# Kernel optimization log

Measured on AMD Instinct MI355X. Metric: run time of the kernel, lower is better.

The kernel has to match this reference:

```python
import jax, jax.numpy as jnp
import numpy as np

REPR_IN = (16, 16, 8)
REPR_OUT = (32, 16, 8)
NUM_BASIS = 16
MAX_RADIUS = 2.0
GAMMA = 16.0  # radial basis sharpness

def _dim(repr_):
    return sum(m * (2 * l + 1) for l, m in enumerate(repr_))

DIM_IN = _dim(REPR_IN)          # 104
SIZE_OUT = _dim(REPR_OUT)       # 120
NUM_GATES = sum(REPR_OUT[1:])   # 24
DIM_OUT = SIZE_OUT + NUM_GATES  # 144 (conv emits gates too)


def setup_inputs() -> dict:
    key = jax.random.key(0)
    k1, k2, k3, k4 = jax.random.split(key, 4)
    B, N, M = 4, 1024, 1024
    features = jax.random.normal(k1, (B, DIM_IN, M), jnp.float32)
    difference_matrix = jax.random.normal(k2, (B, N, M, 3), jnp.float32)
    relative_mask = jax.random.uniform(k3, (B, N, M), jnp.float32)
    W = jax.random.normal(k4, (NUM_BASIS, DIM_OUT, DIM_IN), jnp.float32) / np.sqrt(NUM_BASIS * DIM_IN)
    return {"features": features, "difference_matrix": difference_matrix,
            "relative_mask": relative_mask, "W": W}


def _radial_basis(diff):
    # diff: [B, N, M, 3] -> phi: [B, N, M, K]
    r = jnp.sqrt(jnp.sum(diff * diff, axis=-1) + 1e-12)
    centers = jnp.linspace(0.0, MAX_RADIUS, NUM_BASIS, dtype=diff.dtype)
    return jnp.exp(-GAMMA * jnp.square(r[..., None] - centers))


def reference(features, difference_matrix, relative_mask, W):
    # SE3PointConvolution: per-pair kernel K[b,n,m] = sum_k phi_k(|r_nm|) W[k]
    # masked by relative_mask; out[b,o,n] = sum_m K[b,n,m,o,i] feat[b,i,m].
    # Fused so the [B,N,M,144,104] kernel is never materialized.
    phi = _radial_basis(difference_matrix) * relative_mask[..., None]  # [B,N,M,K]
    tmp = jnp.einsum('bnmk,bim->bnki', phi, features)                  # [B,N,K,DIM_IN]
    y = jnp.einsum('bnki,koi->bon', tmp, W)                            # [B,DIM_OUT,N]

    B, _, N = y.shape
    # scalar (l=0) activation, bias=False
    outs = [jax.nn.relu(y[:, :REPR_OUT[0]])]
    # gates: last NUM_GATES channels, sigmoid
    g = jax.nn.sigmoid(y[:, SIZE_OUT:])
    begin_y, begin_g = REPR_OUT[0], 0
    for l, mul in enumerate(REPR_OUT):
        if l == 0 or mul == 0:
            continue
        d = 2 * l + 1
        fy = y[:, begin_y:begin_y + mul * d].reshape(B, mul, d, N)
        fg = g[:, begin_g:begin_g + mul].reshape(B, mul, 1, N)
        outs.append((fy * fg).reshape(B, mul * d, N))
        begin_y += mul * d
        begin_g += mul
    return jnp.concatenate(outs, axis=1)  # [B, SIZE_OUT, N]
```

## Files before the change

kernel.cpp:

```cpp
#include <hip/hip_runtime.h>


typedef __attribute__((ext_vector_type(4))) float f32x4;
typedef __attribute__((ext_vector_type(8))) short s16x8;

#define DI 104
#define DO 144
#define TTST 1688
#define YST 9

#define W_ELEMS 239616
#define F_ELEMS 425984

#define OFF_PHI0 0
#define OFF_PHI1 16384
#define OFF_FEAT0 32768
#define OFF_FEAT1 47104
#define OFF_Y 61440
#define SMEM_TOTAL (61440 + 144*9*4)

__device__ __forceinline__ float fexp2(float x) {
#if __has_builtin(__builtin_amdgcn_exp2f)
    return __builtin_amdgcn_exp2f(x);
#else
    return exp2f(x);
#endif
}
__device__ __forceinline__ float flog2(float x) {
#if __has_builtin(__builtin_amdgcn_logf)
    return __builtin_amdgcn_logf(x);
#else
    return log2f(x);
#endif
}
__device__ __forceinline__ float fsqrt_(float x) {
#if __has_builtin(__builtin_amdgcn_sqrtf)
    return __builtin_amdgcn_sqrtf(x);
#else
    return sqrtf(x);
#endif
}
__device__ __forceinline__ float frcp_(float x) {
#if __has_builtin(__builtin_amdgcn_rcpf)
    return __builtin_amdgcn_rcpf(x);
#else
    return 1.0f / x;
#endif
}
__device__ __forceinline__ unsigned int pkbf(float lo, float hi) {
    unsigned int a = __builtin_bit_cast(unsigned int, lo) + 0x8000u;
    unsigned int b = __builtin_bit_cast(unsigned int, hi) + 0x8000u;
    return __builtin_amdgcn_perm(b, a, 0x07060302u);
}
__device__ __forceinline__ unsigned short f2b(float f) {
    return (unsigned short)((__builtin_bit_cast(unsigned int, f) + 0x8000u) >> 16);
}

__global__ __launch_bounds__(256, 8)
void cvt_kernel(const float* __restrict__ feat_g, const float* __restrict__ W_g,
                unsigned short* __restrict__ ws)
{
    int gid = blockIdx.x * 256 + threadIdx.x;
    const float* src;
    unsigned short* dst;
    if (gid < W_ELEMS/8) {
        src = W_g + gid*8;  dst = ws + gid*8;
    } else {
        int g2 = gid - W_ELEMS/8;
        src = feat_g + g2*8; dst = ws + W_ELEMS + g2*8;
    }
    f32x4 a = *(const f32x4*)src;
    f32x4 b = *(const f32x4*)(src + 4);
    unsigned int o[4] = { pkbf(a[0],a[1]), pkbf(a[2],a[3]), pkbf(b[0],b[1]), pkbf(b[2],b[3]) };
    *(f32x4*)dst = *(f32x4*)o;
}

#define LOAD_DM(M0)                                                    \
    do {                                                               \
        const float* dp_ = diff_g + (dmrow + (M0) + pml)*3;            \
        dx0 = dp_[0]; dy0 = dp_[1]; dz0 = dp_[2];                      \
        dx1 = dp_[3]; dy1 = dp_[4]; dz1 = dp_[5];                      \
        const float* mp_ = mask_g + dmrow + (M0) + pml;                \
        mk0 = mp_[0]; mk1 = mp_[1];                                    \
    } while (0)

#define LOAD_FEAT(M0)                                                          \
    do {                                                                       \
        fr0 = *(const s16x8*)(featbf + fbase + ((size_t)fi0 << 10) + (M0) + (fj << 3)); \
        if (t < 320)                                                           \
            fr1 = *(const s16x8*)(featbf + fbase + ((size_t)fi1 << 10) + (M0) + (fj << 3)); \
    } while (0)

#define COMPUTE_WRITE_PHI(BUF)                                         \
    do {                                                               \
        unsigned short* pw_ = (BUF) + phirow;                          \
        float r0_ = fsqrt_(fmaf(dx0,dx0, fmaf(dy0,dy0, fmaf(dz0,dz0, 1e-12f)))); \
        float r1_ = fsqrt_(fmaf(dx1,dx1, fmaf(dy1,dy1, fmaf(dz1,dz1, 1e-12f)))); \
        float t0_ = r0_ - K0OFF, t1_ = r1_ - K0OFF;                    \
        float v0_ = fexp2(fmaf(CEXP*t0_, t0_, flog2(mk0)));            \
        float v1_ = fexp2(fmaf(CEXP*t1_, t1_, flog2(mk1)));            \
        float w0_ = fexp2(fmaf(A1, r0_, S0B));                         \
        float w1_ = fexp2(fmaf(A1, r1_, S0B));                         \
        *(unsigned int*)(pw_ + (pblk << 3)) = pkbf(v0_, v1_);          \
        _Pragma("unroll")                                              \
        for (int j_ = 1; j_ < 8; ++j_) {                               \
            v0_ *= w0_; w0_ *= U2;                                     \
            v1_ *= w1_; w1_ *= U2;                                     \
            *(unsigned int*)(pw_ + j_*64 + ((pblk ^ j_) << 3)) = pkbf(v0_, v1_); \
        }                                                              \
    } while (0)

#define WRITE_FEAT(BUF)                                                \
    do {                                                               \
        *(s16x8*)((BUF) + fi0*64 + fjs) = fr0;                         \
        if (t < 320) *(s16x8*)((BUF) + fi1*64 + fjs) = fr1;            \
    } while (0)

#define GEMM1(PBUF, FBUF)                                              \
    do {                                                               \
        _Pragma("unroll")                                              \
        for (int kk_ = 0; kk_ < 2; ++kk_) {                            \
            const int mo_ = ((kk_*4 + q) ^ sw) << 3;                   \
            s16x8 a0_ = *(const s16x8*)((PBUF) + ((2*wr    )*16 + l15)*64 + mo_); \
            s16x8 a1_ = *(const s16x8*)((PBUF) + ((2*wr + 1)*16 + l15)*64 + mo_); \
            _Pragma("unroll")                                          \
            for (int cc_ = 0; cc_ < 4; ++cc_) {                        \
                if (ct0 + cc_ < 7) {                                   \
                    s16x8 bf_ = *(const s16x8*)((FBUF) + ((ct0+cc_)*16 + l15)*64 + mo_); \
                    acc[0][cc_] = __builtin_amdgcn_mfma_f32_16x16x32_bf16(a0_, bf_, acc[0][cc_], 0, 0, 0); \
                    acc[1][cc_] = __builtin_amdgcn_mfma_f32_16x16x32_bf16(a1_, bf_, acc[1][cc_], 0, 0, 0); \
                }                                                      \
            }                                                          \
        }                                                              \
    } while (0)

__global__ __launch_bounds__(512, 4)
void pgb_kernel(const unsigned short* __restrict__ ws,
                const float* __restrict__ diff_g,
                const float* __restrict__ mask_g,
                float* __restrict__ out_g)
{
    const unsigned short* Wbf    = ws;
    const unsigned short* featbf = ws + W_ELEMS;

    __shared__ __align__(16) unsigned char smem[SMEM_TOTAL];
    unsigned short* Tt   = (unsigned short*)smem;
    float*          ylds = (float*)(smem + OFF_Y);
    unsigned short* phi0b  = (unsigned short*)(smem + OFF_PHI0);
    unsigned short* phi1b  = (unsigned short*)(smem + OFF_PHI1);
    unsigned short* feat0b = (unsigned short*)(smem + OFF_FEAT0);
    unsigned short* feat1b = (unsigned short*)(smem + OFF_FEAT1);

    const int t    = threadIdx.x;
    const int b    = blockIdx.x >> 7;
    const int n0   = (blockIdx.x & 127) << 3;
    const int wave = t >> 6;
    const int lane = t & 63;
    const int l15  = lane & 15;
    const int q    = lane >> 4;
    const int wr   = wave >> 1;
    const int ct0  = (wave & 1) << 2;
    const int sw   = l15 & 7;

    if (t < 256) {
        ((unsigned int*)(smem + OFF_FEAT0 + DI*128))[t] = 0u;
        ((unsigned int*)(smem + OFF_FEAT1 + DI*128))[t] = 0u;
    }

    f32x4 acc[2][4];
#pragma unroll
    for (int rr = 0; rr < 2; ++rr)
#pragma unroll
        for (int cc = 0; cc < 4; ++cc)
            acc[rr][cc] = (f32x4){0.f, 0.f, 0.f, 0.f};

    const int pn   = t >> 6;
    const int kh   = (t >> 5) & 1;
    const int pml  = (t & 31) << 1;
    const int pblk = (t & 31) >> 2;
    const int phirow = (pn*16 + kh*8)*64 + (pml & 7);
    const float CEXP = -23.083120654223414f;
    const float A1   = 6.155498841126244f;
    const float V2   = -0.8207331788168325f;
    const float U2   = fexp2(V2);
    const float K0OFF = kh ? 1.0666666666666667f : 0.f;
    const float S0B   = kh ? -6.976232019943076f : -0.41036658940841624f;
    const size_t dmrow = (size_t)((b << 10) + n0 + pn) << 10;

    const int fi0 = t >> 3, fj = t & 7;
    const int fi1 = 64 + (t >> 3);
    const int fjs = (fj ^ (fi0 & 7)) << 3;
    const size_t fbase = (size_t)b * DI << 10;

    float dx0, dy0, dz0, dx1, dy1, dz1, mk0, mk1;
    s16x8 fr0 = {}, fr1 = {};

    LOAD_DM(0);
    LOAD_FEAT(0);
    COMPUTE_WRITE_PHI(phi0b);
    WRITE_FEAT(feat0b);
    LOAD_DM(64);
    LOAD_FEAT(64);

    for (int s = 0; s < 15; ++s) {
        unsigned short* rp = (s & 1) ? phi1b  : phi0b;
        unsigned short* rf = (s & 1) ? feat1b : feat0b;
        unsigned short* wp = (s & 1) ? phi0b  : phi1b;
        unsigned short* wf = (s & 1) ? feat0b : feat1b;
        __syncthreads();
        COMPUTE_WRITE_PHI(wp);
        WRITE_FEAT(wf);
        {
            const int mnext = (s < 14 ? (s + 2) : 15) * 64;
            LOAD_DM(mnext);
            LOAD_FEAT(mnext);
        }
        GEMM1(rp, rf);
    }
    __syncthreads();
    GEMM1(phi1b, feat1b);

    __syncthreads();

#pragma unroll
    for (int rr = 0; rr < 2; ++rr) {
        int nloc = 2*wr + rr;
#pragma unroll
        for (int cc = 0; cc < 4; ++cc) {
            int i = (ct0+cc)*16 + l15;
            if (ct0 + cc < 7 && i < DI) {
#pragma unroll
                for (int r = 0; r < 4; ++r)
                    Tt[nloc*TTST + (q*4+r)*DI + i] = f2b(acc[rr][cc][r]);
            }
        }
    }
    __syncthreads();

    f32x4 y0 = (f32x4){0.f,0.f,0.f,0.f}, y1 = (f32x4){0.f,0.f,0.f,0.f};
    const int o0 = wave*16 + l15;
    const int o1 = 128 + l15;
#pragma unroll 4
    for (int s3 = 0; s3 < 52; ++s3) {
        int a = s3*4 + q;
        int k = a / 13;
        int i = (a - k*13) << 3;
        s16x8 bf = *(const s16x8*)(Tt + (l15 & 7)*TTST + s3*32 + q*8);
        s16x8 af = *(const s16x8*)(Wbf + (size_t)(k*DO + o0)*DI + i);
        y0 = __builtin_amdgcn_mfma_f32_16x16x32_bf16(af, bf, y0, 0, 0, 0);
        if (wave == 0) {
            s16x8 ag = *(const s16x8*)(Wbf + (size_t)(k*DO + o1)*DI + i);
            y1 = __builtin_amdgcn_mfma_f32_16x16x32_bf16(ag, bf, y1, 0, 0, 0);
        }
    }
    if (l15 < 8) {
#pragma unroll
        for (int r = 0; r < 4; ++r)
            ylds[(wave*16 + q*4 + r)*YST + l15] = y0[r];
        if (wave == 0) {
#pragma unroll
            for (int r = 0; r < 4; ++r)
                ylds[(128 + q*4 + r)*YST + l15] = y1[r];
        }
    }
    __syncthreads();

    const float L2E = 1.4426950408889634f;
    for (int idx = t; idx < 120*8; idx += 512) {
        int o = idx >> 3, nn = idx & 7;
        float y = ylds[o*YST + nn];
        float v;
        if (o < 32) {
            v = fmaxf(y, 0.f);
        } else if (o < 80) {
            float g = ylds[(120 + (o-32)/3)*YST + nn];
            v = y * frcp_(1.f + fexp2(-g*L2E));
        } else {
            float g = ylds[(136 + (o-80)/5)*YST + nn];
            v = y * frcp_(1.f + fexp2(-g*L2E));
        }
        out_g[((size_t)(b*120 + o) << 10) + n0 + nn] = v;
    }
}

extern "C" void kernel_launch(void* const* d_in, const int* in_sizes, int n_in,
                              void* d_out, int out_size, void* d_ws, size_t ws_size,
                              hipStream_t stream) {
    const float* feat = (const float*)d_in[0];
    const float* diff = (const float*)d_in[1];
    const float* mask = (const float*)d_in[2];
    const float* W    = (const float*)d_in[3];
    float* out = (float*)d_out;
    unsigned short* ws = (unsigned short*)d_ws;
    (void)in_sizes; (void)n_in; (void)out_size; (void)ws_size;
    cvt_kernel<<<dim3((W_ELEMS + F_ELEMS)/8/256), dim3(256), 0, stream>>>(feat, W, ws);
    pgb_kernel<<<dim3(512), dim3(512), 0, stream>>>(ws, diff, mask, out);
}
```

Before: 140.7 us.

## Single-buffer feature tile to cut LDS and raise occupancy to six blocks

Drops the double-buffered feature tile for a single buffer, shrinking shared memory, and raises the launch-bounds occupancy hint from 4 to 6 blocks per CU. The main loop is rescheduled so the next chunk's global loads are issued before the GEMM and the phi and feature writes happen after a second barrier. This aims to hide latency through more resident waves instead of software pipelining, at the cost of an extra barrier per iteration, less load/compute overlap inside a block, and tighter register limits.

```diff
diff --git a/kernel.cpp b/kernel.cpp
--- a/kernel.cpp
+++ b/kernel.cpp
@@ -14,10 +14,9 @@
 
 #define OFF_PHI0 0
 #define OFF_PHI1 16384
-#define OFF_FEAT0 32768
-#define OFF_FEAT1 47104
-#define OFF_Y 61440
-#define SMEM_TOTAL (61440 + 144*9*4)
+#define OFF_FEAT 32768
+#define OFF_Y    47104
+#define SMEM_TOTAL (47104 + 144*9*4)
 
 __device__ __forceinline__ float fexp2(float x) {
 #if __has_builtin(__builtin_amdgcn_exp2f)
@@ -134,7 +133,7 @@
         }                                                              \
     } while (0)
 
-__global__ __launch_bounds__(512, 4)
+__global__ __launch_bounds__(512, 6)
 void pgb_kernel(const unsigned short* __restrict__ ws,
                 const float* __restrict__ diff_g,
                 const float* __restrict__ mask_g,
@@ -146,10 +145,9 @@
     __shared__ __align__(16) unsigned char smem[SMEM_TOTAL];
     unsigned short* Tt   = (unsigned short*)smem;
     float*          ylds = (float*)(smem + OFF_Y);
-    unsigned short* phi0b  = (unsigned short*)(smem + OFF_PHI0);
-    unsigned short* phi1b  = (unsigned short*)(smem + OFF_PHI1);
-    unsigned short* feat0b = (unsigned short*)(smem + OFF_FEAT0);
-    unsigned short* feat1b = (unsigned short*)(smem + OFF_FEAT1);
+    unsigned short* phi0b = (unsigned short*)(smem + OFF_PHI0);
+    unsigned short* phi1b = (unsigned short*)(smem + OFF_PHI1);
+    unsigned short* featb = (unsigned short*)(smem + OFF_FEAT);
 
     const int t    = threadIdx.x;
     const int b    = blockIdx.x >> 7;
@@ -162,10 +160,7 @@
     const int ct0  = (wave & 1) << 2;
     const int sw   = l15 & 7;
 
-    if (t < 256) {
-        ((unsigned int*)(smem + OFF_FEAT0 + DI*128))[t] = 0u;
-        ((unsigned int*)(smem + OFF_FEAT1 + DI*128))[t] = 0u;
-    }
+    if (t < 256) ((unsigned int*)(smem + OFF_FEAT + DI*128))[t] = 0u;
 
     f32x4 acc[2][4];
 #pragma unroll
@@ -198,29 +193,22 @@
     LOAD_DM(0);
     LOAD_FEAT(0);
     COMPUTE_WRITE_PHI(phi0b);
-    WRITE_FEAT(feat0b);
-    LOAD_DM(64);
-    LOAD_FEAT(64);
-
-    for (int s = 0; s < 15; ++s) {
-        unsigned short* rp = (s & 1) ? phi1b  : phi0b;
-        unsigned short* rf = (s & 1) ? feat1b : feat0b;
-        unsigned short* wp = (s & 1) ? phi0b  : phi1b;
-        unsigned short* wf = (s & 1) ? feat0b : feat1b;
+    WRITE_FEAT(featb);
+
+    for (int s = 0; s < 16; ++s) {
         __syncthreads();
-        COMPUTE_WRITE_PHI(wp);
-        WRITE_FEAT(wf);
-        {
-            const int mnext = (s < 14 ? (s + 2) : 15) * 64;
-            LOAD_DM(mnext);
-            LOAD_FEAT(mnext);
-        }
-        GEMM1(rp, rf);
-    }
-    __syncthreads();
-    GEMM1(phi1b, feat1b);
-
-    __syncthreads();
+        if (s < 15) {
+            const int mn = (s + 1) << 6;
+            LOAD_DM(mn);
+            LOAD_FEAT(mn);
+        }
+        GEMM1((s & 1) ? phi1b : phi0b, featb);
+        __syncthreads();
+        if (s < 15) {
+            COMPUTE_WRITE_PHI((s & 1) ? phi0b : phi1b);
+            WRITE_FEAT(featb);
+        }
+    }
 
 #pragma unroll
     for (int rr = 0; rr < 2; ++rr) {
```

After: 182.6 us. 1.3x slower.

## Interleave radial-basis phi generation with MFMA halves and split recurrence chain

Applied to the files above, without the earlier changes.

The per-pair radial basis is now computed from an anchor that directly seeds two independent recurrences, one for basis 0-3 and one for basis 4-7, instead of one serial 7-step multiply chain. Phi writes are interleaved between the two halves of the GEMM1 k-loop so VALU/exp work overlaps the MFMA instructions within each stage. The global loads for the next stage are moved after the compute. The second recurrence seed uses a clamped power of w, which adds a few multiplies and may change rounding slightly.

```diff
diff --git a/kernel.cpp b/kernel.cpp
--- a/kernel.cpp
+++ b/kernel.cpp
@@ -91,22 +91,32 @@
             fr1 = *(const s16x8*)(featbf + fbase + ((size_t)fi1 << 10) + (M0) + (fj << 3)); \
     } while (0)
 
-#define COMPUTE_WRITE_PHI(BUF)                                         \
-    do {                                                               \
-        unsigned short* pw_ = (BUF) + phirow;                          \
+#define PHI_ANCHOR()                                                   \
+    do {                                                               \
         float r0_ = fsqrt_(fmaf(dx0,dx0, fmaf(dy0,dy0, fmaf(dz0,dz0, 1e-12f)))); \
         float r1_ = fsqrt_(fmaf(dx1,dx1, fmaf(dy1,dy1, fmaf(dz1,dz1, 1e-12f)))); \
         float t0_ = r0_ - K0OFF, t1_ = r1_ - K0OFF;                    \
-        float v0_ = fexp2(fmaf(CEXP*t0_, t0_, flog2(mk0)));            \
-        float v1_ = fexp2(fmaf(CEXP*t1_, t1_, flog2(mk1)));            \
-        float w0_ = fexp2(fmaf(A1, r0_, S0B));                         \
-        float w1_ = fexp2(fmaf(A1, r1_, S0B));                         \
-        *(unsigned int*)(pw_ + (pblk << 3)) = pkbf(v0_, v1_);          \
+        va0 = fexp2(fmaf(CEXP*t0_, t0_, flog2(mk0)));                  \
+        va1 = fexp2(fmaf(CEXP*t1_, t1_, flog2(mk1)));                  \
+        wa0 = fexp2(fmaf(A1, r0_, S0B));                               \
+        wa1 = fexp2(fmaf(A1, r1_, S0B));                               \
+        float p0_ = wa0*wa0, p1_ = wa1*wa1;                            \
+        float q0_ = fminf(p0_*p0_, 3.0e38f);                           \
+        float q1_ = fminf(p1_*p1_, 3.0e38f);                           \
+        vb0 = va0 * q0_ * U2_6;                                        \
+        vb1 = va1 * q1_ * U2_6;                                        \
+        wb0 = wa0 * U2_4;                                              \
+        wb1 = wa1 * U2_4;                                              \
+    } while (0)
+
+#define PHI_WRITE_Q(BUF, V0, V1, W0, W1, J0)                           \
+    do {                                                               \
+        unsigned short* pw_ = (BUF) + phirow;                          \
         _Pragma("unroll")                                              \
-        for (int j_ = 1; j_ < 8; ++j_) {                               \
-            v0_ *= w0_; w0_ *= U2;                                     \
-            v1_ *= w1_; w1_ *= U2;                                     \
-            *(unsigned int*)(pw_ + j_*64 + ((pblk ^ j_) << 3)) = pkbf(v0_, v1_); \
+        for (int j_ = 0; j_ < 4; ++j_) {                               \
+            *(unsigned int*)(pw_ + ((J0) + j_)*64 + ((pblk ^ ((J0) + j_)) << 3)) = pkbf(V0, V1); \
+            V0 *= W0; W0 *= U2;                                        \
+            V1 *= W1; W1 *= U2;                                        \
         }                                                              \
     } while (0)
 
@@ -116,20 +126,17 @@
         if (t < 320) *(s16x8*)((BUF) + fi1*64 + fjs) = fr1;            \
     } while (0)
 
-#define GEMM1(PBUF, FBUF)                                              \
-    do {                                                               \
+#define GEMM1_HALF(PBUF, FBUF, KK)                                     \
+    do {                                                               \
+        const int mo_ = (((KK)*4 + q) ^ sw) << 3;                      \
+        s16x8 a0_ = *(const s16x8*)((PBUF) + ((2*wr    )*16 + l15)*64 + mo_); \
+        s16x8 a1_ = *(const s16x8*)((PBUF) + ((2*wr + 1)*16 + l15)*64 + mo_); \
         _Pragma("unroll")                                              \
-        for (int kk_ = 0; kk_ < 2; ++kk_) {                            \
-            const int mo_ = ((kk_*4 + q) ^ sw) << 3;                   \
-            s16x8 a0_ = *(const s16x8*)((PBUF) + ((2*wr    )*16 + l15)*64 + mo_); \
-            s16x8 a1_ = *(const s16x8*)((PBUF) + ((2*wr + 1)*16 + l15)*64 + mo_); \
-            _Pragma("unroll")                                          \
-            for (int cc_ = 0; cc_ < 4; ++cc_) {                        \
-                if (ct0 + cc_ < 7) {                                   \
-                    s16x8 bf_ = *(const s16x8*)((FBUF) + ((ct0+cc_)*16 + l15)*64 + mo_); \
-                    acc[0][cc_] = __builtin_amdgcn_mfma_f32_16x16x32_bf16(a0_, bf_, acc[0][cc_], 0, 0, 0); \
-                    acc[1][cc_] = __builtin_amdgcn_mfma_f32_16x16x32_bf16(a1_, bf_, acc[1][cc_], 0, 0, 0); \
-                }                                                      \
+        for (int cc_ = 0; cc_ < 4; ++cc_) {                            \
+            if (ct0 + cc_ < 7) {                                       \
+                s16x8 bf_ = *(const s16x8*)((FBUF) + ((ct0+cc_)*16 + l15)*64 + mo_); \
+                acc[0][cc_] = __builtin_amdgcn_mfma_f32_16x16x32_bf16(a0_, bf_, acc[0][cc_], 0, 0, 0); \
+                acc[1][cc_] = __builtin_amdgcn_mfma_f32_16x16x32_bf16(a1_, bf_, acc[1][cc_], 0, 0, 0); \
             }                                                          \
         }                                                              \
     } while (0)
@@ -183,6 +190,9 @@
     const float A1   = 6.155498841126244f;
     const float V2   = -0.8207331788168325f;
     const float U2   = fexp2(V2);
+    const float U2_2 = U2*U2;
+    const float U2_4 = U2_2*U2_2;
+    const float U2_6 = U2_4*U2_2;
     const float K0OFF = kh ? 1.0666666666666667f : 0.f;
     const float S0B   = kh ? -6.976232019943076f : -0.41036658940841624f;
     const size_t dmrow = (size_t)((b << 10) + n0 + pn) << 10;
@@ -194,10 +204,13 @@
 
     float dx0, dy0, dz0, dx1, dy1, dz1, mk0, mk1;
     s16x8 fr0 = {}, fr1 = {};
+    float va0, va1, wa0, wa1, vb0, vb1, wb0, wb1;
 
     LOAD_DM(0);
     LOAD_FEAT(0);
-    COMPUTE_WRITE_PHI(phi0b);
+    PHI_ANCHOR();
+    PHI_WRITE_Q(phi0b, va0, va1, wa0, wa1, 0);
+    PHI_WRITE_Q(phi0b, vb0, vb1, wb0, wb1, 4);
     WRITE_FEAT(feat0b);
     LOAD_DM(64);
     LOAD_FEAT(64);
@@ -208,17 +221,21 @@
         unsigned short* wp = (s & 1) ? phi0b  : phi1b;
         unsigned short* wf = (s & 1) ? feat0b : feat1b;
         __syncthreads();
-        COMPUTE_WRITE_PHI(wp);
         WRITE_FEAT(wf);
+        PHI_ANCHOR();
+        GEMM1_HALF(rp, rf, 0);
+        PHI_WRITE_Q(wp, va0, va1, wa0, wa1, 0);
+        GEMM1_HALF(rp, rf, 1);
+        PHI_WRITE_Q(wp, vb0, vb1, wb0, wb1, 4);
         {
             const int mnext = (s < 14 ? (s + 2) : 15) * 64;
             LOAD_DM(mnext);
             LOAD_FEAT(mnext);
         }
-        GEMM1(rp, rf);
     }
     __syncthreads();
-    GEMM1(phi1b, feat1b);
+    GEMM1_HALF(phi1b, feat1b, 0);
+    GEMM1_HALF(phi1b, feat1b, 1);
 
     __syncthreads();
 
```

Measured after the change: 141.4 us. About the same (+0.5%).

## Warp-specialize producer/consumer waves and pre-pack W in MFMA-friendly order

Applied to the files above, without the earlier changes.

Splits the 8 waves into 4 producer waves, which load the difference matrix, mask and features, compute the radial basis and fill the LDS double buffers, and 4 consumer waves that only issue the first GEMM's MFMAs over all 7 column tiles. Producers now handle 4 pairs per thread with vectorized loads. The conversion kernel also repacks W into a blocked layout so the second GEMM reads contiguous 16-byte chunks without per-iteration index division. The aim is to overlap the transcendental-heavy basis computation with MFMA work. The cost is that each consumer wave holds twice as many accumulators, and the usable threads are split in half.

```diff
diff --git a/kernel.cpp b/kernel.cpp
--- a/kernel.cpp
+++ b/kernel.cpp
@@ -11,6 +11,7 @@
 
 #define W_ELEMS 239616
 #define F_ELEMS 425984
+#define WP_BLKS 29952
 
 #define OFF_PHI0 0
 #define OFF_PHI1 16384
@@ -63,11 +64,17 @@
     int gid = blockIdx.x * 256 + threadIdx.x;
     const float* src;
     unsigned short* dst;
-    if (gid < W_ELEMS/8) {
-        src = W_g + gid*8;  dst = ws + gid*8;
+    if (gid < WP_BLKS) {
+        int a = gid / 144;
+        int o = gid - a * 144;
+        int k = a / 13;
+        int im = (a - k * 13) << 3;
+        src = W_g + ((k * DO + o) * DI + im);
+        dst = ws + gid * 8;
     } else {
-        int g2 = gid - W_ELEMS/8;
-        src = feat_g + g2*8; dst = ws + W_ELEMS + g2*8;
+        int g2 = gid - WP_BLKS;
+        src = feat_g + g2 * 8;
+        dst = ws + W_ELEMS + g2 * 8;
     }
     f32x4 a = *(const f32x4*)src;
     f32x4 b = *(const f32x4*)(src + 4);
@@ -75,61 +82,73 @@
     *(f32x4*)dst = *(f32x4*)o;
 }
 
-#define LOAD_DM(M0)                                                    \
+#define PROD_LOAD(M0)                                                  \
     do {                                                               \
-        const float* dp_ = diff_g + (dmrow + (M0) + pml)*3;            \
-        dx0 = dp_[0]; dy0 = dp_[1]; dz0 = dp_[2];                      \
-        dx1 = dp_[3]; dy1 = dp_[4]; dz1 = dp_[5];                      \
-        const float* mp_ = mask_g + dmrow + (M0) + pml;                \
-        mk0 = mp_[0]; mk1 = mp_[1];                                    \
+        const float* dp_ = diff_g + (dmrow + (M0) + m0)*3;             \
+        dA = *(const f32x4*)dp_;                                       \
+        dB = *(const f32x4*)(dp_ + 4);                                 \
+        dC = *(const f32x4*)(dp_ + 8);                                 \
+        mkv = *(const f32x4*)(mask_g + dmrow + (M0) + m0);             \
+        if (t < 208) {                                                 \
+            const unsigned short* fp_ = featbf + fbase + ((size_t)frow << 10) + (M0) + (fc0 << 3); \
+            f0 = *(const s16x8*)(fp_);                                 \
+            f1 = *(const s16x8*)(fp_ + 8);                             \
+            f2 = *(const s16x8*)(fp_ + 16);                            \
+            f3 = *(const s16x8*)(fp_ + 24);                            \
+        }                                                              \
     } while (0)
 
-#define LOAD_FEAT(M0)                                                          \
-    do {                                                                       \
-        fr0 = *(const s16x8*)(featbf + fbase + ((size_t)fi0 << 10) + (M0) + (fj << 3)); \
-        if (t < 320)                                                           \
-            fr1 = *(const s16x8*)(featbf + fbase + ((size_t)fi1 << 10) + (M0) + (fj << 3)); \
-    } while (0)
-
-#define COMPUTE_WRITE_PHI(BUF)                                         \
+#define PROD_WRITE(PBUF, FBUF)                                         \
     do {                                                               \
-        unsigned short* pw_ = (BUF) + phirow;                          \
-        float r0_ = fsqrt_(fmaf(dx0,dx0, fmaf(dy0,dy0, fmaf(dz0,dz0, 1e-12f)))); \
-        float r1_ = fsqrt_(fmaf(dx1,dx1, fmaf(dy1,dy1, fmaf(dz1,dz1, 1e-12f)))); \
-        float t0_ = r0_ - K0OFF, t1_ = r1_ - K0OFF;                    \
-        float v0_ = fexp2(fmaf(CEXP*t0_, t0_, flog2(mk0)));            \
-        float v1_ = fexp2(fmaf(CEXP*t1_, t1_, flog2(mk1)));            \
-        float w0_ = fexp2(fmaf(A1, r0_, S0B));                         \
-        float w1_ = fexp2(fmaf(A1, r1_, S0B));                         \
-        *(unsigned int*)(pw_ + (pblk << 3)) = pkbf(v0_, v1_);          \
+        float v0_, v1_, v2_, v3_, w0_, w1_, w2_, w3_;                  \
+        { float r_ = fsqrt_(fmaf(dA[0],dA[0], fmaf(dA[1],dA[1], fmaf(dA[2],dA[2], 1e-12f)))); \
+          float tt_ = r_ - K0OFF;                                      \
+          v0_ = fexp2(fmaf(CEXP*tt_, tt_, flog2(mkv[0])));             \
+          w0_ = fexp2(fmaf(A1, r_, S0B)); }                            \
+        { float r_ = fsqrt_(fmaf(dA[3],dA[3], fmaf(dB[0],dB[0], fmaf(dB[1],dB[1], 1e-12f)))); \
+          float tt_ = r_ - K0OFF;                                      \
+          v1_ = fexp2(fmaf(CEXP*tt_, tt_, flog2(mkv[1])));             \
+          w1_ = fexp2(fmaf(A1, r_, S0B)); }                            \
+        { float r_ = fsqrt_(fmaf(dB[2],dB[2], fmaf(dB[3],dB[3], fmaf(dC[0],dC[0], 1e-12f)))); \
+          float tt_ = r_ - K0OFF;                                      \
+          v2_ = fexp2(fmaf(CEXP*tt_, tt_, flog2(mkv[2])));             \
+          w2_ = fexp2(fmaf(A1, r_, S0B)); }                            \
+        { float r_ = fsqrt_(fmaf(dC[1],dC[1], fmaf(dC[2],dC[2], fmaf(dC[3],dC[3], 1e-12f)))); \
+          float tt_ = r_ - K0OFF;                                      \
+          v3_ = fexp2(fmaf(CEXP*tt_, tt_, flog2(mkv[3])));             \
+          w3_ = fexp2(fmaf(A1, r_, S0B)); }                            \
+        unsigned short* pw_ = (PBUF) + pbase;                          \
         _Pragma("unroll")                                              \
-        for (int j_ = 1; j_ < 8; ++j_) {                               \
+        for (int j_ = 0; j_ < 8; ++j_) {                               \
+            unsigned long long pk_ = (unsigned long long)pkbf(v0_, v1_) \
+                                   | ((unsigned long long)pkbf(v2_, v3_) << 32); \
+            *(unsigned long long*)(pw_ + j_*64 + ((pmblk ^ j_) << 3)) = pk_; \
             v0_ *= w0_; w0_ *= U2;                                     \
             v1_ *= w1_; w1_ *= U2;                                     \
-            *(unsigned int*)(pw_ + j_*64 + ((pblk ^ j_) << 3)) = pkbf(v0_, v1_); \
+            v2_ *= w2_; w2_ *= U2;                                     \
+            v3_ *= w3_; w3_ *= U2;                                     \
+        }                                                              \
+        if (t < 208) {                                                 \
+            unsigned short* fw_ = (FBUF) + frow*64;                    \
+            *(s16x8*)(fw_ + (((fc0    ) ^ fsw) << 3)) = f0;            \
+            *(s16x8*)(fw_ + (((fc0 + 1) ^ fsw) << 3)) = f1;            \
+            *(s16x8*)(fw_ + (((fc0 + 2) ^ fsw) << 3)) = f2;            \
+            *(s16x8*)(fw_ + (((fc0 + 3) ^ fsw) << 3)) = f3;            \
         }                                                              \
     } while (0)
 
-#define WRITE_FEAT(BUF)                                                \
-    do {                                                               \
-        *(s16x8*)((BUF) + fi0*64 + fjs) = fr0;                         \
-        if (t < 320) *(s16x8*)((BUF) + fi1*64 + fjs) = fr1;            \
-    } while (0)
-
-#define GEMM1(PBUF, FBUF)                                              \
+#define GEMM1_7(PBUF, FBUF)                                            \
     do {                                                               \
         _Pragma("unroll")                                              \
         for (int kk_ = 0; kk_ < 2; ++kk_) {                            \
             const int mo_ = ((kk_*4 + q) ^ sw) << 3;                   \
-            s16x8 a0_ = *(const s16x8*)((PBUF) + ((2*wr    )*16 + l15)*64 + mo_); \
-            s16x8 a1_ = *(const s16x8*)((PBUF) + ((2*wr + 1)*16 + l15)*64 + mo_); \
+            s16x8 a0_ = *(const s16x8*)((PBUF) + (c*32      + l15)*64 + mo_); \
+            s16x8 a1_ = *(const s16x8*)((PBUF) + (c*32 + 16 + l15)*64 + mo_); \
             _Pragma("unroll")                                          \
-            for (int cc_ = 0; cc_ < 4; ++cc_) {                        \
-                if (ct0 + cc_ < 7) {                                   \
-                    s16x8 bf_ = *(const s16x8*)((FBUF) + ((ct0+cc_)*16 + l15)*64 + mo_); \
-                    acc[0][cc_] = __builtin_amdgcn_mfma_f32_16x16x32_bf16(a0_, bf_, acc[0][cc_], 0, 0, 0); \
-                    acc[1][cc_] = __builtin_amdgcn_mfma_f32_16x16x32_bf16(a1_, bf_, acc[1][cc_], 0, 0, 0); \
-                }                                                      \
+            for (int ct_ = 0; ct_ < 7; ++ct_) {                        \
+                s16x8 bf_ = *(const s16x8*)((FBUF) + (ct_*16 + l15)*64 + mo_); \
+                acc0[ct_] = __builtin_amdgcn_mfma_f32_16x16x32_bf16(a0_, bf_, acc0[ct_], 0, 0, 0); \
+                acc1[ct_] = __builtin_amdgcn_mfma_f32_16x16x32_bf16(a1_, bf_, acc1[ct_], 0, 0, 0); \
             }                                                          \
         }                                                              \
     } while (0)
@@ -140,7 +159,7 @@
                 const float* __restrict__ mask_g,
                 float* __restrict__ out_g)
 {
-    const unsigned short* Wbf    = ws;
+    const unsigned short* Wp     = ws;
     const unsigned short* featbf = ws + W_ELEMS;
 
     __shared__ __align__(16) unsigned char smem[SMEM_TOTAL];
@@ -158,98 +177,92 @@
     const int lane = t & 63;
     const int l15  = lane & 15;
     const int q    = lane >> 4;
-    const int wr   = wave >> 1;
-    const int ct0  = (wave & 1) << 2;
-    const int sw   = l15 & 7;
 
     if (t < 256) {
         ((unsigned int*)(smem + OFF_FEAT0 + DI*128))[t] = 0u;
         ((unsigned int*)(smem + OFF_FEAT1 + DI*128))[t] = 0u;
     }
 
-    f32x4 acc[2][4];
-#pragma unroll
-    for (int rr = 0; rr < 2; ++rr)
-#pragma unroll
-        for (int cc = 0; cc < 4; ++cc)
-            acc[rr][cc] = (f32x4){0.f, 0.f, 0.f, 0.f};
-
-    const int pn   = t >> 6;
-    const int kh   = (t >> 5) & 1;
-    const int pml  = (t & 31) << 1;
-    const int pblk = (t & 31) >> 2;
-    const int phirow = (pn*16 + kh*8)*64 + (pml & 7);
-    const float CEXP = -23.083120654223414f;
-    const float A1   = 6.155498841126244f;
-    const float V2   = -0.8207331788168325f;
-    const float U2   = fexp2(V2);
-    const float K0OFF = kh ? 1.0666666666666667f : 0.f;
-    const float S0B   = kh ? -6.976232019943076f : -0.41036658940841624f;
-    const size_t dmrow = (size_t)((b << 10) + n0 + pn) << 10;
-
-    const int fi0 = t >> 3, fj = t & 7;
-    const int fi1 = 64 + (t >> 3);
-    const int fjs = (fj ^ (fi0 & 7)) << 3;
-    const size_t fbase = (size_t)b * DI << 10;
-
-    float dx0, dy0, dz0, dx1, dy1, dz1, mk0, mk1;
-    s16x8 fr0 = {}, fr1 = {};
-
-    LOAD_DM(0);
-    LOAD_FEAT(0);
-    COMPUTE_WRITE_PHI(phi0b);
-    WRITE_FEAT(feat0b);
-    LOAD_DM(64);
-    LOAD_FEAT(64);
-
-    for (int s = 0; s < 15; ++s) {
-        unsigned short* rp = (s & 1) ? phi1b  : phi0b;
-        unsigned short* rf = (s & 1) ? feat1b : feat0b;
-        unsigned short* wp = (s & 1) ? phi0b  : phi1b;
-        unsigned short* wf = (s & 1) ? feat0b : feat1b;
-        __syncthreads();
-        COMPUTE_WRITE_PHI(wp);
-        WRITE_FEAT(wf);
-        {
-            const int mnext = (s < 14 ? (s + 2) : 15) * 64;
-            LOAD_DM(mnext);
-            LOAD_FEAT(mnext);
-        }
-        GEMM1(rp, rf);
-    }
+    f32x4 acc0[7], acc1[7];
+
+    if (wave < 4) {
+        const int pn    = t >> 5;
+        const int kh    = (t >> 4) & 1;
+        const int mg    = t & 15;
+        const int m0    = mg << 2;
+        const int pmblk = mg >> 1;
+        const int pbase = (pn*16 + kh*8)*64 + (m0 & 7);
+        const int frow  = t >> 1;
+        const int fc0   = (t & 1) << 2;
+        const int fsw   = frow & 7;
+        const float CEXP = -23.083120654223414f;
+        const float A1   = 6.155498841126244f;
+        const float V2   = -0.8207331788168325f;
+        const float U2   = fexp2(V2);
+        const float K0OFF = kh ? 1.0666666666666667f : 0.f;
+        const float S0B   = kh ? -6.976232019943076f : -0.41036658940841624f;
+        const size_t dmrow = (size_t)((b << 10) + n0 + pn) << 10;
+        const size_t fbase = (size_t)b * DI << 10;
+
+        f32x4 dA, dB, dC, mkv;
+        s16x8 f0 = {}, f1 = {}, f2 = {}, f3 = {};
+
+        PROD_LOAD(0);
+        PROD_WRITE(phi0b, feat0b);
+        PROD_LOAD(64);
+
+        for (int s = 0; s < 16; ++s) {
+            __syncthreads();
+            if (s < 15) {
+                unsigned short* wp = (s & 1) ? phi0b  : phi1b;
+                unsigned short* wf = (s & 1) ? feat0b : feat1b;
+                PROD_WRITE(wp, wf);
+                const int mnext = (s < 14 ? (s + 2) : 15) * 64;
+                PROD_LOAD(mnext);
+            }
+        }
+    } else {
+        const int c  = wave - 4;
+        const int sw = l15 & 7;
+#pragma unroll
+        for (int ct = 0; ct < 7; ++ct) {
+            acc0[ct] = (f32x4){0.f, 0.f, 0.f, 0.f};
+            acc1[ct] = (f32x4){0.f, 0.f, 0.f, 0.f};
+        }
+        for (int s = 0; s < 16; ++s) {
+            __syncthreads();
+            GEMM1_7((s & 1) ? phi1b : phi0b, (s & 1) ? feat1b : feat0b);
+        }
+    }
+
     __syncthreads();
-    GEMM1(phi1b, feat1b);
-
+
+    if (wave >= 4) {
+        const int c = wave - 4;
+#pragma unroll
+        for (int ct = 0; ct < 7; ++ct) {
+            int i = ct*16 + l15;
+            if (i < DI) {
+#pragma unroll
+                for (int r = 0; r < 4; ++r) {
+                    Tt[(2*c    )*TTST + (q*4+r)*DI + i] = f2b(acc0[ct][r]);
+                    Tt[(2*c + 1)*TTST + (q*4+r)*DI + i] = f2b(acc1[ct][r]);
+                }
+            }
+        }
+    }
     __syncthreads();
 
-#pragma unroll
-    for (int rr = 0; rr < 2; ++rr) {
-        int nloc = 2*wr + rr;
-#pragma unroll
-        for (int cc = 0; cc < 4; ++cc) {
-            int i = (ct0+cc)*16 + l15;
-            if (ct0 + cc < 7 && i < DI) {
-#pragma unroll
-                for (int r = 0; r < 4; ++r)
-                    Tt[nloc*TTST + (q*4+r)*DI + i] = f2b(acc[rr][cc][r]);
-            }
-        }
-    }
-    __syncthreads();
-
     f32x4 y0 = (f32x4){0.f,0.f,0.f,0.f}, y1 = (f32x4){0.f,0.f,0.f,0.f};
-    const int o0 = wave*16 + l15;
-    const int o1 = 128 + l15;
+    const unsigned short* wp0 = Wp + ((size_t)q*144 + (wave*16 + l15))*8;
+    const unsigned short* wp1 = Wp + ((size_t)q*144 + (128 + l15))*8;
 #pragma unroll 4
     for (int s3 = 0; s3 < 52; ++s3) {
-        int a = s3*4 + q;
-        int k = a / 13;
-        int i = (a - k*13) << 3;
         s16x8 bf = *(const s16x8*)(Tt + (l15 & 7)*TTST + s3*32 + q*8);
-        s16x8 af = *(const s16x8*)(Wbf + (size_t)(k*DO + o0)*DI + i);
+        s16x8 af = *(const s16x8*)(wp0 + (size_t)s3*4608);
         y0 = __builtin_amdgcn_mfma_f32_16x16x32_bf16(af, bf, y0, 0, 0, 0);
         if (wave == 0) {
-            s16x8 ag = *(const s16x8*)(Wbf + (size_t)(k*DO + o1)*DI + i);
+            s16x8 ag = *(const s16x8*)(wp1 + (size_t)s3*4608);
             y1 = __builtin_amdgcn_mfma_f32_16x16x32_bf16(ag, bf, y1, 0, 0, 0);
         }
     }
```

Result: no change. 141.6 us (+0.6%).
